# Performance work log

Hardware: AMD Instinct MI355X
Metric: run time of the kernel (lower is better)

The kernel has to match this reference:

```python
import jax, jax.numpy as jnp
import numpy as np

H, DH, DIM, BNECK, NK, COND = 8, 64, 256, 128, 32, 256


def _ln(x):
    m = x.mean(-1, keepdims=True)
    v = ((x - m) ** 2).mean(-1, keepdims=True)
    return (x - m) * jax.lax.rsqrt(v + 1e-5)


def _mlp(x, w1, b1, w2, b2):
    return jax.nn.gelu(x @ w1 + b1) @ w2 + b2


def _radial(d, w):
    # Bessel-type radial basis sin(n*d)/d projected to heads; limit n as d->0
    n = jnp.arange(1, NK + 1, dtype=d.dtype)
    safe = jnp.maximum(d, 1e-6)[..., None]
    basis = jnp.where(d[..., None] > 1e-6, jnp.sin(d[..., None] * n) / safe, n)
    return jnp.einsum('ijk,kh->hij', basis, w)


def _kernel(x, qk_w):
    # DotProductKernel with softmax=False, scale=1.0
    b, n, _ = x.shape
    qk = (x @ qk_w).reshape(b, n, 2, H, DH).transpose(0, 3, 2, 1, 4)  # b h two n d
    q, k = qk[:, :, 0], qk[:, :, 1]
    return jnp.einsum('bhid,bhjd->bhij', q, k)


def reference(u, lat, lat_diff, lon_diff, scalar_cond, adaLN_w, adaLN_b, to_v_w, to_x_in_w, to_x_w1, to_x_b1, to_x_w2, to_x_b2, to_y_in_w, to_y_w1, to_y_b1, to_y_w2, to_y_b2, kx_qk_w, ky_qk_w, rx_w, ry_w, merge_w, merge_b, ffn_w1, ffn_b1, ffn_w2, ffn_b2):
    b, nlat, nlon, c = u.shape
    mod = (scalar_cond @ adaLN_w + adaLN_b)[:, None, None]  # (b,1,1,6c)
    sh_msa, sc_msa, g_msa, sh_mlp, sc_mlp, g_mlp = jnp.split(mod, 6, axis=-1)
    u_skip = u
    um = _ln(u) * (1 + sc_msa) + sh_msa  # modulate_fused
    lw = jnp.cos(lat)
    lw = lw / lw.mean()
    # PoolingReducer over lat (weighted) -> (b, nlon, bneck)
    u_x = _mlp(jnp.einsum('bilc,cd,i->bld', um, to_x_in_w, lw) / nlat,
               to_x_w1, to_x_b1, to_x_w2, to_x_b2)
    # PoolingReducer over lon -> (b, nlat, bneck)
    u_y = _mlp((um @ to_y_in_w).mean(axis=2), to_y_w1, to_y_b1, to_y_w2, to_y_b2)
    k_x = jax.nn.softmax(_kernel(u_x, kx_qk_w) * _radial(lon_diff, rx_w)[None], axis=-1)
    k_y = jax.nn.softmax(_kernel(u_y, ky_qk_w) * _radial(lat_diff, ry_w)[None], axis=-1)
    v = (um @ to_v_w).reshape(b, nlat, nlon, H, DH).transpose(0, 3, 1, 2, 4)  # b h i l c
    u_phi = jnp.einsum('bhij,bhjmc->bhimc', k_y, v)
    u_phi = jnp.einsum('bhlm,bhimc->bhilc', k_x, u_phi)
    u_phi = u_phi.transpose(0, 2, 3, 1, 4)  # b i l h c
    mu = u_phi.mean(-1, keepdims=True)
    var = ((u_phi - mu) ** 2).mean(-1, keepdims=True)
    gn = ((u_phi - mu) * jax.lax.rsqrt(var + 1e-6)).reshape(b, nlat, nlon, H * DH)
    u1 = u_skip + g_msa * (gn @ merge_w + merge_b)  # bias_dropout_add_scale (inference)
    u2 = _ln(u1) * (1 + sc_mlp) + sh_mlp
    return u1 + g_mlp * _mlp(u2, ffn_w1, ffn_b1, ffn_w2, ffn_b2)


def setup_inputs():
    key = jax.random.key(0)
    ks = jax.random.split(key, 20)
    b, nlat, nlon = 4, 128, 256
    dim, h, dh, bn, cond = DIM, H, DH, BNECK, COND
    f = jnp.float32
    u = jax.random.normal(ks[0], (b, nlat, nlon, dim), f)
    lat = jnp.linspace(-np.pi / 2 + 0.01, np.pi / 2 - 0.01, nlat).astype(f)
    lat_diff = jnp.abs(lat[:, None] - lat[None, :])
    lon = (jnp.arange(nlon) * (2 * np.pi / nlon)).astype(f)
    d = jnp.abs(lon[:, None] - lon[None, :])
    lon_diff = jnp.minimum(d, 2 * np.pi - d)
    scalar_cond = jax.random.normal(ks[1], (b, cond), f)

    def w(k, shape, s=0.02):
        return jax.random.normal(k, shape, f) * s

    return dict(
        u=u, lat=lat, lat_diff=lat_diff, lon_diff=lon_diff, scalar_cond=scalar_cond,
        adaLN_w=w(ks[2], (cond, 6 * dim)), adaLN_b=w(ks[3], (6 * dim,)),
        to_v_w=w(ks[4], (dim, h * dh)),
        to_x_in_w=w(ks[5], (dim, dim)), to_x_w1=w(ks[6], (dim, dim)), to_x_b1=jnp.zeros((dim,), f),
        to_x_w2=w(ks[7], (dim, bn)), to_x_b2=jnp.zeros((bn,), f),
        to_y_in_w=w(ks[8], (dim, dim)), to_y_w1=w(ks[9], (dim, dim)), to_y_b1=jnp.zeros((dim,), f),
        to_y_w2=w(ks[10], (dim, bn)), to_y_b2=jnp.zeros((bn,), f),
        kx_qk_w=w(ks[11], (bn, 2 * h * dh)), ky_qk_w=w(ks[12], (bn, 2 * h * dh)),
        rx_w=w(ks[13], (NK, h), 0.1), ry_w=w(ks[14], (NK, h), 0.1),
        merge_w=w(ks[15], (h * dh, dim)), merge_b=jnp.zeros((dim,), f),
        ffn_w1=w(ks[16], (dim, 4 * dim)), ffn_b1=jnp.zeros((4 * dim,), f),
        ffn_w2=w(ks[17], (4 * dim, dim)), ffn_b2=jnp.zeros((dim,), f))
```

## Files before the change

### kernel.cpp

```cpp
#include <hip/hip_runtime.h>
#include <hip/hip_bf16.h>
#include <math.h>


#define B_ 4
#define NLAT 128
#define NLON 256
#define NTOK (B_*NLAT*NLON)
#define SLOT_ELE ((size_t)16777216)

typedef __hip_bfloat16 bf16;
typedef unsigned short u16;
typedef __attribute__((ext_vector_type(8))) short short8;
typedef __attribute__((ext_vector_type(4))) float f32x4;

__device__ __forceinline__ float b2f(bf16 x){ return __bfloat162float(x); }
__device__ __forceinline__ bf16  f2b(float x){ return __float2bfloat16(x); }
__device__ __forceinline__ u16 f2bits(float x){
  bf16 h = __float2bfloat16(x); return *(u16*)&h;
}
__device__ __forceinline__ float bits2f(u16 u){
  union { unsigned int i; float f; } v; v.i = ((unsigned int)u) << 16; return v.f;
}
__device__ __forceinline__ float gelu_f(float x){
  float x3 = x*x*x;
  return 0.5f*x*(1.0f + tanhf(0.7978845608028654f*(x + 0.044715f*x3)));
}
__device__ __forceinline__ float gelu_fast(float x){
  float t = 0.7978845608028654f*(x + 0.044715f*x*x*x);
  float e = __builtin_amdgcn_exp2f(t * 2.8853900817779268f);
  return x - x*__builtin_amdgcn_rcpf(e + 1.0f);
}
__device__ __forceinline__ float ldin(const void* p, size_t i, int flag){
  return flag ? b2f(((const bf16*)p)[i]) : ((const float*)p)[i];
}
__device__ __forceinline__ short4 pack4(float a, float b, float c, float d){
  short4 r; r.x = (short)f2bits(a); r.y = (short)f2bits(b);
  r.z = (short)f2bits(c); r.w = (short)f2bits(d); return r;
}
__device__ __forceinline__ short8 pack8(float a, float b, float c, float d,
                                        float e, float f, float g, float h){
  short8 r;
  r[0]=(short)f2bits(a); r[1]=(short)f2bits(b); r[2]=(short)f2bits(c); r[3]=(short)f2bits(d);
  r[4]=(short)f2bits(e); r[5]=(short)f2bits(f); r[6]=(short)f2bits(g); r[7]=(short)f2bits(h);
  return r;
}
__device__ __forceinline__ void stage16(const u16* g, u16* l){
  __builtin_amdgcn_global_load_lds(
      (const __attribute__((address_space(1))) void*)g,
      (__attribute__((address_space(3))) void*)l, 16, 0, 0);
}

__global__ void k_detect(const void* lon_diff, int* flag){
  const float c = 0.02454369260617026f;
  float asF = ((const float*)lon_diff)[1];
  float asB = b2f(((const bf16*)lon_diff)[1]);
  float ef = fabsf(asF - c), eb = fabsf(asB - c);
  if (!isfinite(ef)) ef = 1e30f;
  *flag = (eb < ef) ? 1 : 0;
}

__global__ __launch_bounds__(256) void k_cvt(const void* __restrict__ src,
                                             float* __restrict__ dst, int n,
                                             const int* __restrict__ flag){
  int f = *flag;
  for (int i = blockIdx.x*256 + threadIdx.x; i < n; i += gridDim.x*256)
    dst[i] = ldin(src, i, f);
}

__global__ __launch_bounds__(256) void k_wprep(const float* __restrict__ W,
                                               u16* __restrict__ wf,
                                               int KS, int ldn, int total){
  int gid = blockIdx.x*256 + threadIdx.x;
  if (gid >= total) return;
  int j = gid & 7; int lane = (gid >> 3) & 63; int rest = gid >> 9;
  int ks = rest % KS; int nt = rest / KS;
  int k = ks*32 + (lane >> 4)*8 + j;
  int n = nt*16 + (lane & 15);
  wf[gid] = f2bits(W[(size_t)k*ldn + n]);
}

__global__ __launch_bounds__(256) void k_wprep2(const float* __restrict__ W,
                                                u16* __restrict__ wf){
  int gid = blockIdx.x*256 + threadIdx.x;
  int j = gid & 7; int lane = (gid >> 3) & 63; int rest = gid >> 9;
  int nt = rest & 15; int ksAll = rest >> 4;
  int k = ksAll*32 + (lane >> 4)*8 + j;
  int n = nt*16 + (lane & 15);
  wf[gid] = f2bits(W[(size_t)k*256 + n]);
}

__global__ __launch_bounds__(256) void k_wtrans(const float* __restrict__ W,
                                                u16* __restrict__ WT, int K, int N){
  int gid = blockIdx.x*256 + threadIdx.x;
  if (gid >= K*N) return;
  int k = gid % K, n = gid / K;
  WT[(size_t)n*K + k] = f2bits(W[(size_t)k*N + n]);
}

__global__ __launch_bounds__(256) void k_mod(const float* __restrict__ sc,
                                             const float* __restrict__ w,
                                             const float* __restrict__ bias,
                                             float* __restrict__ mod){
  int gid = blockIdx.x*256 + threadIdx.x;
  int s = gid / 1536, j = gid % 1536;
  float acc = bias[j];
  for (int c = 0; c < 256; ++c) acc += sc[s*256+c] * w[c*1536+j];
  mod[gid] = acc;
}

__global__ __launch_bounds__(128) void k_lw(const float* __restrict__ lat,
                                            float* __restrict__ lw){
  __shared__ float red[128];
  int i = threadIdx.x;
  float cv = cosf(lat[i]);
  red[i] = cv; __syncthreads();
  for (int s = 64; s > 0; s >>= 1){ if (i < s) red[i] += red[i+s]; __syncthreads(); }
  float mean = red[0] * (1.0f/128.0f);
  lw[i] = cv / mean;
}

__global__ __launch_bounds__(256) void k_um2(const void* __restrict__ u,
                                             const float* __restrict__ mod,
                                             u16* __restrict__ um,
                                             const int* __restrict__ flag){
  __shared__ u16 tile[64][264];
  __shared__ float r1[64][4], r2[64][4], mv[64], rs[64];
  __shared__ float ssh[256], ssc[256];
  int f = *flag; int tid = threadIdx.x;
  int t0 = blockIdx.x*64; int b = t0 >> 15;
  ssh[tid] = mod[b*1536 + tid];
  ssc[tid] = mod[b*1536 + 256 + tid];
  for (int it = 0; it < 16; ++it){
    int idx = it*256 + tid;
    int tok = idx >> 6, c4 = idx & 63;
    short4 v4;
    if (f){
      v4 = *(const short4*)((const bf16*)u + ((size_t)(t0+tok))*256 + c4*4);
    } else {
      float4 fv = ((const float4*)u)[((size_t)(t0+tok))*64 + c4];
      v4 = pack4(fv.x, fv.y, fv.z, fv.w);
    }
    *(short4*)&tile[tok][c4*4] = v4;
  }
  __syncthreads();
  {
    int tok = tid >> 2, part = tid & 3;
    float s1 = 0.f, s2 = 0.f;
    for (int c4 = 0; c4 < 16; ++c4){
      short4 v4 = *(const short4*)&tile[tok][part*64 + c4*4];
      float a = bits2f((u16)v4.x), bb = bits2f((u16)v4.y),
            c = bits2f((u16)v4.z), d = bits2f((u16)v4.w);
      s1 += a+bb+c+d; s2 += a*a+bb*bb+c*c+d*d;
    }
    r1[tok][part] = s1; r2[tok][part] = s2;
  }
  __syncthreads();
  if ((tid & 3) == 0){
    int tok = tid >> 2;
    float a1 = r1[tok][0]+r1[tok][1]+r1[tok][2]+r1[tok][3];
    float a2 = r2[tok][0]+r2[tok][1]+r2[tok][2]+r2[tok][3];
    float mean = a1*(1.0f/256.0f);
    float var = a2*(1.0f/256.0f) - mean*mean;
    mv[tok] = mean; rs[tok] = rsqrtf(var + 1e-5f);
  }
  __syncthreads();
  for (int it = 0; it < 16; ++it){
    int idx = it*256 + tid;
    int tok = idx >> 6, c4 = idx & 63;
    float mean = mv[tok], rstd = rs[tok];
    short4 v4 = *(const short4*)&tile[tok][c4*4];
    float y[4]; u16 raw[4] = {(u16)v4.x,(u16)v4.y,(u16)v4.z,(u16)v4.w};
    #pragma unroll
    for (int p = 0; p < 4; ++p){
      int c = c4*4 + p;
      y[p] = (bits2f(raw[p]) - mean)*rstd*(1.0f + ssc[c]) + ssh[c];
    }
    *(short4*)(um + ((size_t)(t0+tok))*256 + c4*4) = pack4(y[0],y[1],y[2],y[3]);
  }
}

__global__ __launch_bounds__(256) void k_redx(const u16* __restrict__ um,
                                              const float* __restrict__ lw,
                                              float* __restrict__ redx){
  __shared__ float lws[128];
  int tid = threadIdx.x;
  if (tid < 128) lws[tid] = lw[tid];
  __syncthreads();
  int gid = blockIdx.x*256 + tid;
  int c = gid & 255; int l = (gid >> 8) & 255; int b = gid >> 16;
  float acc = 0.0f;
  for (int i = 0; i < 128; ++i)
    acc += bits2f(um[(((size_t)(b*128 + i)*256 + l)*256) + c]) * lws[i];
  redx[gid] = acc * (1.0f/128.0f);
}

__global__ __launch_bounds__(256) void k_redy(const u16* __restrict__ um,
                                              float* __restrict__ redy){
  int gid = blockIdx.x*256 + threadIdx.x;
  int c = gid & 255; int i = (gid >> 8) & 127; int b = gid >> 15;
  float acc = 0.0f;
  for (int l = 0; l < 256; ++l)
    acc += bits2f(um[(((size_t)(b*128 + i)*256 + l)*256) + c]);
  redy[gid] = acc * (1.0f/256.0f);
}

__global__ __launch_bounds__(256) void gemm_row2(
    const float* __restrict__ Ax, const float* __restrict__ Wx,
    const float* __restrict__ bx, float* __restrict__ Cx, int Kx, int Nx,
    const float* __restrict__ Ay, const float* __restrict__ Wy,
    const float* __restrict__ by, float* __restrict__ Cy, int Ky, int Ny,
    int nbx, int act){
  __shared__ float As[256];
  int bid = blockIdx.x; int tid = threadIdx.x;
  const float* A; const float* W; const float* bias; float* C; int K, N, r;
  if (bid < nbx){ A=Ax; W=Wx; bias=bx; C=Cx; K=Kx; N=Nx; r=bid; }
  else          { A=Ay; W=Wy; bias=by; C=Cy; K=Ky; N=Ny; r=bid-nbx; }
  for (int k = tid; k < K; k += 256) As[k] = A[(size_t)r*K + k];
  __syncthreads();
  for (int n = tid; n < N; n += 256){
    float a0=0.f, a1=0.f, a2=0.f, a3=0.f;
    for (int k = 0; k < K; k += 4){
      a0 += As[k+0]*W[(size_t)(k+0)*N + n];
      a1 += As[k+1]*W[(size_t)(k+1)*N + n];
      a2 += As[k+2]*W[(size_t)(k+2)*N + n];
      a3 += As[k+3]*W[(size_t)(k+3)*N + n];
    }
    float acc = (a0+a1)+(a2+a3) + (bias ? bias[n] : 0.0f);
    if (act == 1) acc = gelu_f(acc);
    C[(size_t)r*N + n] = acc;
  }
}

__global__ __launch_bounds__(256) void k_radial(const float* __restrict__ d,
                                                const float* __restrict__ w,
                                                float* __restrict__ rad, int n){
  int gid = blockIdx.x*256 + threadIdx.x;
  int nn = n*n;
  int h = gid / nn; int rem = gid % nn;
  float dv = d[rem];
  float safe = fmaxf(dv, 1e-6f);
  float acc = 0.0f;
  for (int k = 0; k < 32; ++k){
    float nk = (float)(k+1);
    float basis = (dv > 1e-6f) ? (sinf(dv*nk)/safe) : nk;
    acc += basis * w[k*8 + h];
  }
  rad[gid] = acc;
}

__global__ __launch_bounds__(256) void k_qkT(const float* __restrict__ qk,
                                             float* __restrict__ kT, int n){
  int gid = blockIdx.x*256 + threadIdx.x;
  int j = gid % n; int rest = gid / n;
  int d = rest & 63; int bh = rest >> 6;
  int b = bh >> 3, h = bh & 7;
  kT[gid] = qk[((size_t)(b*n + j))*1024 + 512 + h*64 + d];
}

__global__ __launch_bounds__(256) void k_attn2(const float* __restrict__ qk,
                                               const float* __restrict__ kT,
                                               const float* __restrict__ rad,
                                               u16* __restrict__ kout, int n){
  extern __shared__ float sm[];
  float* qs = sm; float* red = sm + 64;
  int j = threadIdx.x;
  int bid = blockIdx.x; int i = bid % n; int h = (bid / n) & 7; int b = bid / (n*8);
  if (j < 64) qs[j] = qk[((size_t)(b*n + i))*1024 + h*64 + j];
  __syncthreads();
  const float* kcol = kT + ((size_t)((b*8 + h)*64))*n + j;
  float dot = 0.0f;
  #pragma unroll 8
  for (int d0 = 0; d0 < 64; ++d0) dot += qs[d0]*kcol[(size_t)d0*n];
  float s = dot * rad[((size_t)(h*n + i))*n + j];
  float m = s;
  #pragma unroll
  for (int off = 32; off; off >>= 1) m = fmaxf(m, __shfl_xor(m, off));
  int wv = j >> 6, nw = n >> 6;
  if ((j & 63) == 0) red[wv] = m;
  __syncthreads();
  m = red[0];
  for (int w = 1; w < nw; ++w) m = fmaxf(m, red[w]);
  float e = __builtin_amdgcn_exp2f((s - m)*1.44269504088896f);
  float t = e;
  #pragma unroll
  for (int off = 32; off; off >>= 1) t += __shfl_xor(t, off);
  if ((j & 63) == 0) red[4 + wv] = t;
  __syncthreads();
  t = 0.0f;
  for (int w = 0; w < nw; ++w) t += red[4 + w];
  kout[(size_t)bid*n + j] = f2bits(e / t);
}

__global__ __launch_bounds__(256) void k_v2(const u16* __restrict__ um,
                                            const u16* __restrict__ WvT,
                                            u16* __restrict__ vT,
                                            int b0, size_t bstr){
  int tid = threadIdx.x;
  int wave = tid>>6, lane = tid&63, quad = lane>>4, l15 = lane&15;
  int bid = blockIdx.x;
  int b = b0 + (bid >> 9);
  int t0 = (bid & 511)*64;
  u16* vTb = vT + (size_t)(b - b0)*bstr;
  const u16* umb = um + ((size_t)b*32768 + t0)*256;
  f32x4 acc[8][4];
  #pragma unroll
  for (int mt = 0; mt < 8; ++mt)
    #pragma unroll
    for (int nt = 0; nt < 4; ++nt) acc[mt][nt] = (f32x4){0.f,0.f,0.f,0.f};
  for (int ks = 0; ks < 8; ++ks){
    short8 bfr[4];
    #pragma unroll
    for (int nt = 0; nt < 4; ++nt)
      bfr[nt] = *(const short8*)(umb + (size_t)(nt*16 + l15)*256 + ks*32 + quad*8);
    #pragma unroll
    for (int mt = 0; mt < 8; ++mt){
      short8 a = *(const short8*)(WvT + (size_t)((wave*8+mt)*16 + l15)*256 + ks*32 + quad*8);
      #pragma unroll
      for (int nt = 0; nt < 4; ++nt)
        acc[mt][nt] = __builtin_amdgcn_mfma_f32_16x16x32_bf16(a, bfr[nt], acc[mt][nt], 0, 0, 0);
    }
  }
  #pragma unroll
  for (int mt = 0; mt < 8; ++mt){
    int hc0 = (wave*8+mt)*16 + quad*4;
    int h = hc0 >> 6, c0 = hc0 & 63;
    #pragma unroll
    for (int nt = 0; nt < 4; ++nt){
      int tok = t0 + nt*16 + l15;
      *(short4*)(vTb + (size_t)h*2097152 + (size_t)tok*64 + c0)
        = pack4(acc[mt][nt][0], acc[mt][nt][1], acc[mt][nt][2], acc[mt][nt][3]);
    }
  }
}

__global__ __launch_bounds__(256) void k_phi1b(const u16* __restrict__ kyb,
                                               const u16* __restrict__ vT,
                                               u16* __restrict__ phi,
                                               int b0, size_t bstr){
  int tid = threadIdx.x;
  int wave = tid>>6, lane = tid&63, quad = lane>>4, l15 = lane&15;
  int bid = blockIdx.x;
  int b = b0 + (bid >> 9);
  int rem = bid & 511; int mblk = rem & 63, h = rem >> 6;
  int m0 = mblk*256;
  const u16* vTh = vT + (size_t)(b - b0)*bstr + (size_t)h*2097152;
  u16* phib = phi + (size_t)(b - b0)*bstr;
  const u16* kyh = kyb + (size_t)(b*8+h)*16384;
  f32x4 acc[4][8];
  #pragma unroll
  for (int mt = 0; mt < 4; ++mt)
    #pragma unroll
    for (int nt = 0; nt < 8; ++nt) acc[mt][nt] = (f32x4){0.f,0.f,0.f,0.f};
  for (int ks = 0; ks < 4; ++ks){
    short8 bfr[8];
    #pragma unroll
    for (int nt = 0; nt < 8; ++nt)
      bfr[nt] = *(const short8*)(kyh + (size_t)(nt*16 + l15)*128 + ks*32 + quad*8);
    #pragma unroll
    for (int mt = 0; mt < 4; ++mt){
      int cm = m0 + (wave*4+mt)*16 + l15;
      int c = cm >> 8, m = cm & 255;
      const u16* gp = vTh + ((size_t)(ks*32 + quad*8)*256 + m)*64 + c;
      short8 a;
      #pragma unroll
      for (int jj = 0; jj < 8; ++jj) ((u16*)&a)[jj] = gp[(size_t)jj*16384];
      #pragma unroll
      for (int nt = 0; nt < 8; ++nt)
        acc[mt][nt] = __builtin_amdgcn_mfma_f32_16x16x32_bf16(a, bfr[nt], acc[mt][nt], 0, 0, 0);
    }
  }
  #pragma unroll
  for (int mt = 0; mt < 4; ++mt){
    int cmr = m0 + (wave*4+mt)*16 + quad*4;
    #pragma unroll
    for (int nt = 0; nt < 8; ++nt){
      int i = nt*16 + l15;
      *(short4*)(phib + (size_t)h*2097152 + (size_t)i*16384 + cmr)
        = pack4(acc[mt][nt][0], acc[mt][nt][1], acc[mt][nt][2], acc[mt][nt][3]);
    }
  }
}

__global__ __launch_bounds__(256) void k_phi2b(const u16* __restrict__ kxb,
                                               const u16* __restrict__ phi,
                                               u16* __restrict__ OUTt,
                                               int b0, size_t bstr){
  int tid = threadIdx.x;
  int wave = tid>>6, lane = tid&63, quad = lane>>4, l15 = lane&15;
  int bid = blockIdx.x;
  int b = b0 + (bid >> 9);
  int rem = bid & 511; int mblk = rem & 63, h = rem >> 6;
  int m0 = mblk*128;
  int mhalf = (wave&1)*4, nhalf = (wave>>1)*8;
  const u16* ph = phi + (size_t)(b - b0)*bstr + (size_t)h*2097152;
  u16* OUTb = OUTt + (size_t)(b - b0)*bstr;
  const u16* kxh = kxb + (size_t)(b*8+h)*65536;
  f32x4 acc[4][8];
  #pragma unroll
  for (int mt = 0; mt < 4; ++mt)
    #pragma unroll
    for (int nt = 0; nt < 8; ++nt) acc[mt][nt] = (f32x4){0.f,0.f,0.f,0.f};
  for (int ks = 0; ks < 8; ++ks){
    short8 bfr[8];
    #pragma unroll
    for (int nt = 0; nt < 8; ++nt)
      bfr[nt] = *(const short8*)(kxh + (size_t)((nhalf+nt)*16 + l15)*256 + ks*32 + quad*8);
    #pragma unroll
    for (int mt = 0; mt < 4; ++mt){
      int m2 = m0 + (mhalf+mt)*16 + l15;
      short8 a = *(const short8*)(ph + (size_t)m2*256 + ks*32 + quad*8);
      #pragma unroll
      for (int nt = 0; nt < 8; ++nt)
        acc[mt][nt] = __builtin_amdgcn_mfma_f32_16x16x32_bf16(a, bfr[nt], acc[mt][nt], 0, 0, 0);
    }
  }
  #pragma unroll
  for (int mt = 0; mt < 4; ++mt){
    int m2r = m0 + (mhalf+mt)*16 + quad*4;
    #pragma unroll
    for (int nt = 0; nt < 8; ++nt){
      int l = (nhalf+nt)*16 + l15;
      *(short4*)(OUTb + (size_t)h*2097152 + (size_t)l*8192 + m2r)
        = pack4(acc[mt][nt][0], acc[mt][nt][1], acc[mt][nt][2], acc[mt][nt][3]);
    }
  }
}

__global__ __launch_bounds__(256) void k_gnb(const u16* __restrict__ OUTt,
                                             u16* __restrict__ gn,
                                             int b0, size_t bstr){
  int tid = threadIdx.x;
  int bid = blockIdx.x;
  int bi = bid >> 11;
  int rem = bid & 2047; int l = rem & 255, h = rem >> 8;
  int i = tid >> 1, half = tid & 1;
  const u16* src = OUTt + (size_t)bi*bstr + (size_t)h*2097152 + (size_t)l*8192 + i*64 + half*32;
  float v[32]; float s1 = 0.f, s2 = 0.f;
  #pragma unroll
  for (int c4 = 0; c4 < 8; ++c4){
    short4 v4 = *(const short4*)(src + c4*4);
    v[c4*4+0] = bits2f((u16)v4.x); v[c4*4+1] = bits2f((u16)v4.y);
    v[c4*4+2] = bits2f((u16)v4.z); v[c4*4+3] = bits2f((u16)v4.w);
  }
  #pragma unroll
  for (int c = 0; c < 32; ++c){ s1 += v[c]; s2 += v[c]*v[c]; }
  s1 += __shfl_xor(s1, 1); s2 += __shfl_xor(s2, 1);
  float mean = s1*(1.0f/64.0f);
  float var = s2*(1.0f/64.0f) - mean*mean;
  float rstd = rsqrtf(var + 1e-6f);
  u16* dst = gn + (size_t)bi*bstr + ((size_t)(i*256 + l))*512 + h*64 + half*32;
  #pragma unroll
  for (int c4 = 0; c4 < 8; ++c4)
    *(short4*)(dst + c4*4) = pack4((v[c4*4+0]-mean)*rstd, (v[c4*4+1]-mean)*rstd,
                                   (v[c4*4+2]-mean)*rstd, (v[c4*4+3]-mean)*rstd);
}

__global__ __launch_bounds__(256) void k_mergeb(const u16* __restrict__ gn,
                                                const u16* __restrict__ WmT,
                                                const float* __restrict__ biasm,
                                                const float* __restrict__ mod,
                                                const void* __restrict__ u,
                                                void* __restrict__ outv,
                                                const int* __restrict__ flag,
                                                int b0, size_t bstr){
  __shared__ float smg[256], sbb[256];
  int f = *flag;
  int tid = threadIdx.x;
  int bid = blockIdx.x;
  int b = b0 + (bid >> 8);
  int t0 = (bid & 255)*128;
  smg[tid] = mod[b*1536 + 512 + tid];
  sbb[tid] = biasm[tid];
  __syncthreads();
  int wave = tid>>6, lane = tid&63, quad = lane>>4, l15 = lane&15;
  const u16* gnb = gn + (size_t)(b - b0)*bstr;
  int nt0 = wave*2;
  f32x4 acc[16][2];
  #pragma unroll
  for (int mt = 0; mt < 16; ++mt){ acc[mt][0] = (f32x4){0.f,0.f,0.f,0.f}; acc[mt][1] = (f32x4){0.f,0.f,0.f,0.f}; }
  for (int ks = 0; ks < 16; ++ks){
    short8 bfr[2];
    #pragma unroll
    for (int nti = 0; nti < 2; ++nti){
      int tok = t0 + (nt0+nti)*16 + l15;
      bfr[nti] = *(const short8*)(gnb + (size_t)tok*512 + ks*32 + quad*8);
    }
    #pragma unroll
    for (int mt = 0; mt < 16; ++mt){
      short8 a = *(const short8*)(WmT + (size_t)(mt*16 + l15)*512 + ks*32 + quad*8);
      #pragma unroll
      for (int nti = 0; nti < 2; ++nti)
        acc[mt][nti] = __builtin_amdgcn_mfma_f32_16x16x32_bf16(a, bfr[nti], acc[mt][nti], 0, 0, 0);
    }
  }
  #pragma unroll
  for (int mt = 0; mt < 16; ++mt){
    int d0 = mt*16 + quad*4;
    #pragma unroll
    for (int nti = 0; nti < 2; ++nti){
      int tok = t0 + (nt0+nti)*16 + l15;
      size_t o = ((size_t)b*32768 + tok)*256 + d0;
      float r0,r1,r2,r3;
      if (f){
        short4 rv = *(const short4*)((const bf16*)u + o);
        r0 = bits2f((u16)rv.x); r1 = bits2f((u16)rv.y); r2 = bits2f((u16)rv.z); r3 = bits2f((u16)rv.w);
      } else {
        float4 rv = *(const float4*)((const float*)u + o);
        r0 = rv.x; r1 = rv.y; r2 = rv.z; r3 = rv.w;
      }
      float y0 = r0 + smg[d0+0]*(acc[mt][nti][0] + sbb[d0+0]);
      float y1 = r1 + smg[d0+1]*(acc[mt][nti][1] + sbb[d0+1]);
      float y2 = r2 + smg[d0+2]*(acc[mt][nti][2] + sbb[d0+2]);
      float y3 = r3 + smg[d0+3]*(acc[mt][nti][3] + sbb[d0+3]);
      if (f) *(short4*)((bf16*)outv + o) = pack4(y0,y1,y2,y3);
      else   *(float4*)((float*)outv + o) = (float4){y0,y1,y2,y3};
    }
  }
}

__global__ __launch_bounds__(256, 2) void k_ffn4(
    const float* __restrict__ mod,
    const u16* __restrict__ w1f,
    const float* __restrict__ b1c,
    const u16* __restrict__ w2f,
    const float* __restrict__ b2c,
    void* __restrict__ outv,
    const int* __restrict__ flag){
  __shared__ __align__(16) u16 wbuf[2][16384];
  __shared__ __align__(16) u16 hs[64][40];
  int f = *flag;
  int tid = threadIdx.x;
  int wave = tid>>6, lane = tid&63, quad = lane>>4, l15 = lane&15;
  int mrow = wave*16;
  int t0 = blockIdx.x*64;
  int bb = t0 >> 15;
  const float* modp = mod + bb*1536;
  size_t rowbase = ((size_t)(t0 + mrow + l15))*256;

  {
    #pragma unroll
    for (int i = 0; i < 8; ++i){
      int seg = wave*8 + i;
      const u16* src = (seg < 16)
          ? (w1f + (size_t)seg*512 + lane*8)
          : (w2f + (size_t)(seg-16)*512 + lane*8);
      stage16(src, &wbuf[0][seg*512]);
    }
  }

  short8 afr[8];
  float s1 = 0.f, s2 = 0.f;
  #pragma unroll
  for (int ks = 0; ks < 8; ++ks){
    int c0 = ks*32 + quad*8;
    float v0,v1,v2,v3,v4,v5,v6,v7;
    if (f){
      short8 r = *(const short8*)((const bf16*)outv + rowbase + c0);
      afr[ks] = r;
      v0 = bits2f((u16)r[0]); v1 = bits2f((u16)r[1]); v2 = bits2f((u16)r[2]); v3 = bits2f((u16)r[3]);
      v4 = bits2f((u16)r[4]); v5 = bits2f((u16)r[5]); v6 = bits2f((u16)r[6]); v7 = bits2f((u16)r[7]);
    } else {
      float4 fa = *(const float4*)((const float*)outv + rowbase + c0);
      float4 fb = *(const float4*)((const float*)outv + rowbase + c0 + 4);
      v0=fa.x; v1=fa.y; v2=fa.z; v3=fa.w; v4=fb.x; v5=fb.y; v6=fb.z; v7=fb.w;
      afr[ks] = pack8(v0,v1,v2,v3,v4,v5,v6,v7);
    }
    s1 += v0+v1+v2+v3+v4+v5+v6+v7;
    s2 += v0*v0+v1*v1+v2*v2+v3*v3+v4*v4+v5*v5+v6*v6+v7*v7;
  }
  s1 += __shfl_xor(s1, 16); s1 += __shfl_xor(s1, 32);
  s2 += __shfl_xor(s2, 16); s2 += __shfl_xor(s2, 32);
  float mean = s1*(1.0f/256.0f);
  float var = s2*(1.0f/256.0f) - mean*mean;
  float rstd = rsqrtf(var + 1e-5f);
  #pragma unroll
  for (int ks = 0; ks < 8; ++ks){
    int c0 = ks*32 + quad*8;
    float4 sh0 = *(const float4*)&modp[768 + c0];
    float4 sh1 = *(const float4*)&modp[768 + c0 + 4];
    float4 sc0 = *(const float4*)&modp[1024 + c0];
    float4 sc1 = *(const float4*)&modp[1024 + c0 + 4];
    short8 r = afr[ks];
    float y0 = (bits2f((u16)r[0]) - mean)*rstd*(1.0f+sc0.x) + sh0.x;
    float y1 = (bits2f((u16)r[1]) - mean)*rstd*(1.0f+sc0.y) + sh0.y;
    float y2 = (bits2f((u16)r[2]) - mean)*rstd*(1.0f+sc0.z) + sh0.z;
    float y3 = (bits2f((u16)r[3]) - mean)*rstd*(1.0f+sc0.w) + sh0.w;
    float y4 = (bits2f((u16)r[4]) - mean)*rstd*(1.0f+sc1.x) + sh1.x;
    float y5 = (bits2f((u16)r[5]) - mean)*rstd*(1.0f+sc1.y) + sh1.y;
    float y6 = (bits2f((u16)r[6]) - mean)*rstd*(1.0f+sc1.z) + sh1.z;
    float y7 = (bits2f((u16)r[7]) - mean)*rstd*(1.0f+sc1.w) + sh1.w;
    afr[ks] = pack8(y0,y1,y2,y3,y4,y5,y6,y7);
  }

  __syncthreads();

  f32x4 acc2[16];
  #pragma unroll
  for (int nt = 0; nt < 16; ++nt) acc2[nt] = (f32x4){0.f,0.f,0.f,0.f};
  int buf = 0;
  #pragma unroll 1
  for (int c = 0; c < 32; ++c){
    if (c < 31){
      int cn = c + 1;
      #pragma unroll
      for (int i = 0; i < 8; ++i){
        int seg = wave*8 + i;
        const u16* src = (seg < 16)
            ? (w1f + (size_t)cn*8192 + (size_t)seg*512 + lane*8)
            : (w2f + (size_t)cn*8192 + (size_t)(seg-16)*512 + lane*8);
        stage16(src, &wbuf[buf^1][seg*512]);
      }
    }
    const u16* w1l = &wbuf[buf][0];
    const u16* w2l = &wbuf[buf][8192];
    f32x4 acc1[2];
    acc1[0] = (f32x4){0.f,0.f,0.f,0.f}; acc1[1] = (f32x4){0.f,0.f,0.f,0.f};
    #pragma unroll
    for (int ks = 0; ks < 8; ++ks){
      #pragma unroll
      for (int nt2 = 0; nt2 < 2; ++nt2){
        short8 bfr = *(const short8*)(w1l + (nt2*8 + ks)*512 + lane*8);
        acc1[nt2] = __builtin_amdgcn_mfma_f32_16x16x32_bf16(afr[ks], bfr, acc1[nt2], 0, 0, 0);
      }
    }
    __builtin_amdgcn_sched_barrier(0);
    #pragma unroll
    for (int nt2 = 0; nt2 < 2; ++nt2){
      int hid = nt2*16 + l15;
      float b1 = b1c[c*32 + hid];
      #pragma unroll
      for (int r = 0; r < 4; ++r)
        hs[mrow + quad*4 + r][hid] = f2bits(gelu_fast(acc1[nt2][r] + b1));
    }
    __builtin_amdgcn_sched_barrier(0);
    asm volatile("s_waitcnt lgkmcnt(0)" ::: "memory");
    __builtin_amdgcn_sched_barrier(0);
    short8 a2 = *(const short8*)&hs[mrow + l15][quad*8];
    #pragma unroll
    for (int nt = 0; nt < 16; ++nt){
      short8 bfr = *(const short8*)(w2l + nt*512 + lane*8);
      acc2[nt] = __builtin_amdgcn_mfma_f32_16x16x32_bf16(a2, bfr, acc2[nt], 0, 0, 0);
    }
    __syncthreads();
    buf ^= 1;
  }

  #pragma unroll
  for (int nt = 0; nt < 16; ++nt){
    int col = nt*16 + l15;
    float g = modp[1280 + col];
    float b2v = b2c[col];
    #pragma unroll
    for (int r = 0; r < 4; ++r){
      size_t o = ((size_t)(t0 + mrow + quad*4 + r))*256 + col;
      float resid = f ? bits2f(((const u16*)outv)[o]) : ((const float*)outv)[o];
      float y = resid + g*(acc2[nt][r] + b2v);
      if (f) ((u16*)outv)[o] = f2bits(y);
      else   ((float*)outv)[o] = y;
    }
  }
}

extern "C" void kernel_launch(void* const* d_in, const int* in_sizes, int n_in,
                              void* d_out, int out_size, void* d_ws, size_t ws_size,
                              hipStream_t stream){
  (void)n_in; (void)out_size;

  char* p = (char*)d_ws;
  auto alloc = [&](size_t bytes)->void*{
    void* r = (void*)p; p += (bytes + 255) & ~(size_t)255; return r;
  };

  int* flag = (int*)alloc(4);
  float* cin[28];
  cin[0] = nullptr;
  for (int i = 1; i < 28; ++i) cin[i] = (float*)alloc((size_t)in_sizes[i]*4);

  float* mod  = (float*)alloc((size_t)4*1536*4);
  float* lw   = (float*)alloc((size_t)128*4);
  float* redx = (float*)alloc((size_t)4*256*256*4);
  float* redy = (float*)alloc((size_t)4*128*256*4);
  float* tx   = (float*)alloc((size_t)4*256*256*4);
  float* hx   = (float*)alloc((size_t)4*256*256*4);
  float* uxb  = (float*)alloc((size_t)4*256*128*4);
  float* ty   = (float*)alloc((size_t)4*128*256*4);
  float* hy   = (float*)alloc((size_t)4*128*256*4);
  float* uyb  = (float*)alloc((size_t)4*128*128*4);
  float* qkx  = (float*)alloc((size_t)4*256*1024*4);
  float* qky  = (float*)alloc((size_t)4*128*1024*4);
  float* kTx  = (float*)alloc((size_t)4*8*64*256*4);
  float* kTy  = (float*)alloc((size_t)4*8*64*128*4);
  float* radx = (float*)alloc((size_t)8*256*256*4);
  float* rady = (float*)alloc((size_t)8*128*128*4);
  u16* kxb = (u16*)alloc((size_t)32*256*256*2);
  u16* kyb = (u16*)alloc((size_t)32*128*128*2);
  u16* w1f = (u16*)alloc((size_t)256*1024*2);
  u16* w2f = (u16*)alloc((size_t)1024*256*2);
  u16* WvT = (u16*)alloc((size_t)512*256*2);
  u16* WmT = (u16*)alloc((size_t)256*512*2);
  u16* um  = (u16*)alloc((size_t)NTOK*256*2);

  size_t used = (size_t)(p - (char*)d_ws);
  int merged = (ws_size > used) && ((ws_size - used) >= (size_t)8*SLOT_ELE*2 + 65536);
  size_t slotBytes = (merged ? 4 : 1) * SLOT_ELE * 2;
  u16* slotV = (u16*)alloc(slotBytes);
  u16* slotP = (u16*)alloc(slotBytes);

  const void* u = d_in[0];

  k_detect<<<1, 1, 0, stream>>>(d_in[3], flag);
  for (int i = 1; i < 28; ++i){
    int n = in_sizes[i];
    int blocks = (n + 255)/256; if (blocks > 1024) blocks = 1024;
    k_cvt<<<blocks, 256, 0, stream>>>(d_in[i], cin[i], n, flag);
  }
  k_wprep<<<1024, 256, 0, stream>>>(cin[24], w1f, 8, 1024, 256*1024);
  k_wprep2<<<1024, 256, 0, stream>>>(cin[26], w2f);
  k_wtrans<<<512, 256, 0, stream>>>(cin[7],  WvT, 256, 512);
  k_wtrans<<<512, 256, 0, stream>>>(cin[22], WmT, 512, 256);

  k_mod<<<24, 256, 0, stream>>>(cin[4], cin[5], cin[6], mod);
  k_lw<<<1, 128, 0, stream>>>(cin[1], lw);
  k_um2<<<NTOK/64, 256, 0, stream>>>(u, mod, um, flag);
  k_redx<<<1024, 256, 0, stream>>>(um, lw, redx);
  k_redy<<<512, 256, 0, stream>>>(um, redy);
  gemm_row2<<<1536, 256, 0, stream>>>(redx, cin[8],  nullptr,  tx,  256, 256,
                                      redy, cin[13], nullptr,  ty,  256, 256, 1024, 0);
  gemm_row2<<<1536, 256, 0, stream>>>(tx,   cin[9],  cin[10],  hx,  256, 256,
                                      ty,   cin[14], cin[15],  hy,  256, 256, 1024, 1);
  gemm_row2<<<1536, 256, 0, stream>>>(hx,   cin[11], cin[12],  uxb, 256, 128,
                                      hy,   cin[16], cin[17],  uyb, 256, 128, 1024, 0);
  gemm_row2<<<1536, 256, 0, stream>>>(uxb,  cin[18], nullptr,  qkx, 128, 1024,
                                      uyb,  cin[19], nullptr,  qky, 128, 1024, 1024, 0);
  k_radial<<<(8*256*256)/256, 256, 0, stream>>>(cin[3], cin[20], radx, 256);
  k_radial<<<(8*128*128)/256, 256, 0, stream>>>(cin[2], cin[21], rady, 128);
  k_qkT<<<2048, 256, 0, stream>>>(qkx, kTx, 256);
  k_qkT<<<1024, 256, 0, stream>>>(qky, kTy, 128);
  k_attn2<<<4*8*256, 256, (64+8)*4, stream>>>(qkx, kTx, radx, kxb, 256);
  k_attn2<<<4*8*128, 128, (64+8)*4, stream>>>(qky, kTy, rady, kyb, 128);

  if (merged){
    k_v2    <<<2048, 256, 0, stream>>>(um, WvT, slotV, 0, SLOT_ELE);
    k_phi1b <<<2048, 256, 0, stream>>>(kyb, slotV, slotP, 0, SLOT_ELE);
    k_phi2b <<<2048, 256, 0, stream>>>(kxb, slotP, slotV, 0, SLOT_ELE);
    k_gnb   <<<8192, 256, 0, stream>>>(slotV, slotP, 0, SLOT_ELE);
    k_mergeb<<<1024, 256, 0, stream>>>(slotP, WmT, cin[23], mod, u, d_out, flag, 0, SLOT_ELE);
  } else {
    for (int b = 0; b < 4; ++b){
      k_v2    <<<512, 256, 0, stream>>>(um, WvT, slotV, b, 0);
      k_phi1b <<<512, 256, 0, stream>>>(kyb, slotV, slotP, b, 0);
      k_phi2b <<<512, 256, 0, stream>>>(kxb, slotP, slotV, b, 0);
      k_gnb   <<<2048, 256, 0, stream>>>(slotV, slotP, b, 0);
      k_mergeb<<<256, 256, 0, stream>>>(slotP, WmT, cin[23], mod, u, d_out, flag, b, 0);
    }
  }
  k_ffn4<<<NTOK/64, 256, 0, stream>>>(mod, w1f, cin[25], w2f, cin[27], d_out, flag);
}
```

Before: 1.796 ms.

## Store V in lat-contiguous layout via LDS transpose; batch input conversions into one launch

The V projection kernel now tiles over (lon, lat-block) and transposes its output through shared memory, so V is stored with the lat index contiguous. The first contraction can then load its A operand as a single 16-byte vector instead of eight strided 2-byte gathers. Separately, the 27 per-input conversion launches are replaced by one kernel that walks a table of cumulative offsets. The costs are extra LDS traffic, lower occupancy in the V kernel, strided token reads from um, and a per-element linear search over the offset table.

New measurement: 1.452 ms. 1.24x faster.

```diff
diff --git a/kernel.cpp b/kernel.cpp
--- a/kernel.cpp
+++ b/kernel.cpp
@@ -60,12 +60,20 @@
   *flag = (eb < ef) ? 1 : 0;
 }
 
-__global__ __launch_bounds__(256) void k_cvt(const void* __restrict__ src,
-                                             float* __restrict__ dst, int n,
-                                             const int* __restrict__ flag){
+struct CvtTab {
+  const void* src[27];
+  float* dst[27];
+  int cum[28];
+};
+__global__ __launch_bounds__(256) void k_cvtall(CvtTab t, const int* __restrict__ flag,
+                                                int total){
   int f = *flag;
-  for (int i = blockIdx.x*256 + threadIdx.x; i < n; i += gridDim.x*256)
-    dst[i] = ldin(src, i, f);
+  for (int i = blockIdx.x*256 + threadIdx.x; i < total; i += gridDim.x*256){
+    int s = 0;
+    while (i >= t.cum[s+1]) ++s;
+    int off = i - t.cum[s];
+    t.dst[s][off] = ldin(t.src[s], off, f);
+  }
 }
 
 __global__ __launch_bounds__(256) void k_wprep(const float* __restrict__ W,
@@ -292,17 +300,18 @@
   kout[(size_t)bid*n + j] = f2bits(e / t);
 }
 
-__global__ __launch_bounds__(256) void k_v2(const u16* __restrict__ um,
-                                            const u16* __restrict__ WvT,
-                                            u16* __restrict__ vT,
-                                            int b0, size_t bstr){
+__global__ __launch_bounds__(256, 2) void k_v3(const u16* __restrict__ um,
+                                               const u16* __restrict__ WvT,
+                                               u16* __restrict__ vA,
+                                               int b0, size_t bstr){
+  __shared__ __align__(16) u16 T[512][72];
   int tid = threadIdx.x;
   int wave = tid>>6, lane = tid&63, quad = lane>>4, l15 = lane&15;
   int bid = blockIdx.x;
   int b = b0 + (bid >> 9);
-  int t0 = (bid & 511)*64;
-  u16* vTb = vT + (size_t)(b - b0)*bstr;
-  const u16* umb = um + ((size_t)b*32768 + t0)*256;
+  int rem = bid & 511;
+  int m = rem & 255, jt = rem >> 8;
+  const u16* umb = um + ((size_t)b*32768)*256;
   f32x4 acc[8][4];
   #pragma unroll
   for (int mt = 0; mt < 8; ++mt)
@@ -311,8 +320,10 @@
   for (int ks = 0; ks < 8; ++ks){
     short8 bfr[4];
     #pragma unroll
-    for (int nt = 0; nt < 4; ++nt)
-      bfr[nt] = *(const short8*)(umb + (size_t)(nt*16 + l15)*256 + ks*32 + quad*8);
+    for (int nt = 0; nt < 4; ++nt){
+      int j = jt*64 + nt*16 + l15;
+      bfr[nt] = *(const short8*)(umb + ((size_t)j*256 + m)*256 + ks*32 + quad*8);
+    }
     #pragma unroll
     for (int mt = 0; mt < 8; ++mt){
       short8 a = *(const short8*)(WvT + (size_t)((wave*8+mt)*16 + l15)*256 + ks*32 + quad*8);
@@ -324,18 +335,28 @@
   #pragma unroll
   for (int mt = 0; mt < 8; ++mt){
     int hc0 = (wave*8+mt)*16 + quad*4;
-    int h = hc0 >> 6, c0 = hc0 & 63;
     #pragma unroll
     for (int nt = 0; nt < 4; ++nt){
-      int tok = t0 + nt*16 + l15;
-      *(short4*)(vTb + (size_t)h*2097152 + (size_t)tok*64 + c0)
-        = pack4(acc[mt][nt][0], acc[mt][nt][1], acc[mt][nt][2], acc[mt][nt][3]);
-    }
-  }
-}
-
-__global__ __launch_bounds__(256) void k_phi1b(const u16* __restrict__ kyb,
-                                               const u16* __restrict__ vT,
+      int jp = nt*16 + l15;
+      T[hc0+0][jp] = f2bits(acc[mt][nt][0]);
+      T[hc0+1][jp] = f2bits(acc[mt][nt][1]);
+      T[hc0+2][jp] = f2bits(acc[mt][nt][2]);
+      T[hc0+3][jp] = f2bits(acc[mt][nt][3]);
+    }
+  }
+  __syncthreads();
+  u16* vAb = vA + (size_t)(b - b0)*bstr;
+  for (int it = 0; it < 16; ++it){
+    int idx = it*256 + tid;
+    int g = idx & 7, hc = idx >> 3;
+    short8 v8 = *(const short8*)&T[hc][g*8];
+    int h = hc >> 6, c = hc & 63;
+    *(short8*)(vAb + (size_t)h*2097152 + ((size_t)c*256 + m)*128 + jt*64 + g*8) = v8;
+  }
+}
+
+__global__ __launch_bounds__(256) void k_phi1c(const u16* __restrict__ kyb,
+                                               const u16* __restrict__ vA,
                                                u16* __restrict__ phi,
                                                int b0, size_t bstr){
   int tid = threadIdx.x;
@@ -344,7 +365,7 @@
   int b = b0 + (bid >> 9);
   int rem = bid & 511; int mblk = rem & 63, h = rem >> 6;
   int m0 = mblk*256;
-  const u16* vTh = vT + (size_t)(b - b0)*bstr + (size_t)h*2097152;
+  const u16* vAh = vA + (size_t)(b - b0)*bstr + (size_t)h*2097152;
   u16* phib = phi + (size_t)(b - b0)*bstr;
   const u16* kyh = kyb + (size_t)(b*8+h)*16384;
   f32x4 acc[4][8];
@@ -360,11 +381,7 @@
     #pragma unroll
     for (int mt = 0; mt < 4; ++mt){
       int cm = m0 + (wave*4+mt)*16 + l15;
-      int c = cm >> 8, m = cm & 255;
-      const u16* gp = vTh + ((size_t)(ks*32 + quad*8)*256 + m)*64 + c;
-      short8 a;
-      #pragma unroll
-      for (int jj = 0; jj < 8; ++jj) ((u16*)&a)[jj] = gp[(size_t)jj*16384];
+      short8 a = *(const short8*)(vAh + (size_t)cm*128 + ks*32 + quad*8);
       #pragma unroll
       for (int nt = 0; nt < 8; ++nt)
         acc[mt][nt] = __builtin_amdgcn_mfma_f32_16x16x32_bf16(a, bfr[nt], acc[mt][nt], 0, 0, 0);
@@ -710,10 +727,17 @@
   const void* u = d_in[0];
 
   k_detect<<<1, 1, 0, stream>>>(d_in[3], flag);
-  for (int i = 1; i < 28; ++i){
-    int n = in_sizes[i];
-    int blocks = (n + 255)/256; if (blocks > 1024) blocks = 1024;
-    k_cvt<<<blocks, 256, 0, stream>>>(d_in[i], cin[i], n, flag);
+  {
+    CvtTab t;
+    int cum = 0;
+    for (int i = 1; i < 28; ++i){
+      t.src[i-1] = d_in[i];
+      t.dst[i-1] = cin[i];
+      t.cum[i-1] = cum;
+      cum += in_sizes[i];
+    }
+    t.cum[27] = cum;
+    k_cvtall<<<2048, 256, 0, stream>>>(t, flag, cum);
   }
   k_wprep<<<1024, 256, 0, stream>>>(cin[24], w1f, 8, 1024, 256*1024);
   k_wprep2<<<1024, 256, 0, stream>>>(cin[26], w2f);
@@ -741,15 +765,15 @@
   k_attn2<<<4*8*128, 128, (64+8)*4, stream>>>(qky, kTy, rady, kyb, 128);
 
   if (merged){
-    k_v2    <<<2048, 256, 0, stream>>>(um, WvT, slotV, 0, SLOT_ELE);
-    k_phi1b <<<2048, 256, 0, stream>>>(kyb, slotV, slotP, 0, SLOT_ELE);
+    k_v3    <<<2048, 256, 0, stream>>>(um, WvT, slotV, 0, SLOT_ELE);
+    k_phi1c <<<2048, 256, 0, stream>>>(kyb, slotV, slotP, 0, SLOT_ELE);
     k_phi2b <<<2048, 256, 0, stream>>>(kxb, slotP, slotV, 0, SLOT_ELE);
     k_gnb   <<<8192, 256, 0, stream>>>(slotV, slotP, 0, SLOT_ELE);
     k_mergeb<<<1024, 256, 0, stream>>>(slotP, WmT, cin[23], mod, u, d_out, flag, 0, SLOT_ELE);
   } else {
     for (int b = 0; b < 4; ++b){
-      k_v2    <<<512, 256, 0, stream>>>(um, WvT, slotV, b, 0);
-      k_phi1b <<<512, 256, 0, stream>>>(kyb, slotV, slotP, b, 0);
+      k_v3    <<<512, 256, 0, stream>>>(um, WvT, slotV, b, 0);
+      k_phi1c <<<512, 256, 0, stream>>>(kyb, slotV, slotP, b, 0);
       k_phi2b <<<512, 256, 0, stream>>>(kxb, slotP, slotV, b, 0);
       k_gnb   <<<2048, 256, 0, stream>>>(slotV, slotP, b, 0);
       k_mergeb<<<256, 256, 0, stream>>>(slotP, WmT, cin[23], mod, u, d_out, flag, b, 0);
```
